# Optimization experiments

Measured on AMD Instinct MI355X. Metric: run time of the kernel, lower is better.

The kernel has to match this reference:

```python
import jax, jax.numpy as jnp
import numpy as np

N = 1_000_000       # total nodes
B = 4096            # number of graphs (batch_size)
D = 128             # in_channels
T = 3               # processing_steps
EPS = 1e-16         # torch_geometric softmax denominator epsilon


def setup_inputs() -> dict:
    key = jax.random.key(0)
    k0, k1, k2, k3, k4, k5 = jax.random.split(key, 6)
    x = jax.random.normal(k0, (N, D), dtype=jnp.float32)
    batch = jnp.sort(jax.random.randint(k1, (N,), 0, B, dtype=jnp.int32))
    # GRU params (input size 2D, hidden size D); scaled like orthogonal-ish init
    s = 1.0 / np.sqrt(D)
    w_ih = jax.random.normal(k2, (3 * D, 2 * D), dtype=jnp.float32) * s
    w_hh = jax.random.normal(k3, (3 * D, D), dtype=jnp.float32) * s
    b_ih = jax.random.normal(k4, (3 * D,), dtype=jnp.float32) * s
    b_hh = jax.random.normal(k5, (3 * D,), dtype=jnp.float32) * s
    return {"x": x, "batch": batch, "w_ih": w_ih, "w_hh": w_hh,
            "b_ih": b_ih, "b_hh": b_hh}


def _gru_cell(inp, h, w_ih, w_hh, b_ih, b_hh):
    # PyTorch GRU cell: gates ordered (r, z, n)
    gi = inp @ w_ih.T + b_ih          # [B, 3D]
    gh = h @ w_hh.T + b_hh            # [B, 3D]
    i_r, i_z, i_n = jnp.split(gi, 3, axis=-1)
    h_r, h_z, h_n = jnp.split(gh, 3, axis=-1)
    r = jax.nn.sigmoid(i_r + h_r)
    z = jax.nn.sigmoid(i_z + h_z)
    n = jnp.tanh(i_n + r * h_n)
    return (1.0 - z) * n + z * h


def reference(x, batch, w_ih, w_hh, b_ih, b_hh):
    h = jnp.zeros((B, D), dtype=x.dtype)
    q_star = jnp.zeros((B, 2 * D), dtype=x.dtype)
    for _ in range(T):  # small fixed number of processing steps
        h = _gru_cell(q_star, h, w_ih, w_hh, b_ih, b_hh)
        q = h                                           # [B, D]
        e = jnp.sum(x * q[batch], axis=-1)              # [N] dot scores
        # segment softmax over each graph's nodes
        m = jax.ops.segment_max(e, batch, num_segments=B)
        ex = jnp.exp(e - m[batch])
        s = jax.ops.segment_sum(ex, batch, num_segments=B)
        a = ex / (s[batch] + EPS)                       # [N]
        r_pool = jax.ops.segment_sum(a[:, None] * x, batch, num_segments=B)  # [B, D]
        q_star = jnp.concatenate([q, r_pool], axis=-1)  # [B, 2D]
    return q_star
```

## Files before the change

kernel.cpp:

```cpp
#include <hip/hip_runtime.h>
#include <hip/hip_bf16.h>
#include <math.h>

#define NB 4096
#define DD 128
#define TT 3

__global__ void transpose_w(const float* __restrict__ w, float* __restrict__ wt,
                            int R, int C) {
    int idx = blockIdx.x * blockDim.x + threadIdx.x;
    if (idx >= R * C) return;
    int r = idx % R;
    int c = idx / R;
    wt[idx] = w[r * C + c];
}

__global__ void seg_starts(const int* __restrict__ batch, int* __restrict__ seg,
                           int N, int B) {
    int i = blockIdx.x * blockDim.x + threadIdx.x;
    if (i >= N) return;
    int bi = batch[i];
    int bp = (i == 0) ? -1 : batch[i - 1];
    for (int b = bp + 1; b <= bi; ++b) seg[b] = i;
    if (i == N - 1) {
        for (int b = bi + 1; b <= B; ++b) seg[b] = N;
    }
}

__global__ __launch_bounds__(256) void gru_kernel(
    const float* qstar_in, const float* h_in,
    const float* __restrict__ wt_ih, const float* __restrict__ wt_hh,
    const float* __restrict__ b_ih, const float* __restrict__ b_hh,
    float* h_out, float* qstar_out ) {

    __shared__ float qs[16 * 256];
    __shared__ float hs[16 * 128];

    const int tid = threadIdx.x;
    const int b0  = blockIdx.x * 16;

    const float* qsrc = qstar_in + (size_t)b0 * 256;
    for (int t = tid; t < 16 * 256; t += 256) qs[t] = qsrc[t];
    const float* hsrc = h_in + (size_t)b0 * 128;
    for (int t = tid; t < 16 * 128; t += 256) hs[t] = hsrc[t];
    __syncthreads();

    const int j  = tid & 127;
    const int gb = (tid >> 7) * 8;

    float air[8], aiz[8], ain[8], ahr[8], ahz[8], ahn[8];
    const float br = b_ih[j], bz = b_ih[128 + j], bn = b_ih[256 + j];
    const float cr = b_hh[j], cz = b_hh[128 + j], cn = b_hh[256 + j];
#pragma unroll
    for (int g = 0; g < 8; ++g) {
        air[g] = br; aiz[g] = bz; ain[g] = bn;
        ahr[g] = cr; ahz[g] = cz; ahn[g] = cn;
    }

#pragma unroll 4
    for (int k = 0; k < 256; ++k) {
        const float wr = wt_ih[k * 384 + j];
        const float wz = wt_ih[k * 384 + 128 + j];
        const float wn = wt_ih[k * 384 + 256 + j];
#pragma unroll
        for (int g = 0; g < 8; ++g) {
            const float qv = qs[(gb + g) * 256 + k];
            air[g] = fmaf(qv, wr, air[g]);
            aiz[g] = fmaf(qv, wz, aiz[g]);
            ain[g] = fmaf(qv, wn, ain[g]);
        }
    }
#pragma unroll 4
    for (int k = 0; k < 128; ++k) {
        const float wr = wt_hh[k * 384 + j];
        const float wz = wt_hh[k * 384 + 128 + j];
        const float wn = wt_hh[k * 384 + 256 + j];
#pragma unroll
        for (int g = 0; g < 8; ++g) {
            const float hv = hs[(gb + g) * 128 + k];
            ahr[g] = fmaf(hv, wr, ahr[g]);
            ahz[g] = fmaf(hv, wz, ahz[g]);
            ahn[g] = fmaf(hv, wn, ahn[g]);
        }
    }

#pragma unroll
    for (int g = 0; g < 8; ++g) {
        const int gg = gb + g;
        const float r = 1.f / (1.f + __expf(-(air[g] + ahr[g])));
        const float z = 1.f / (1.f + __expf(-(aiz[g] + ahz[g])));
        const float n = tanhf(ain[g] + r * ahn[g]);
        const float hv = hs[gg * 128 + j];
        const float hnew = (1.f - z) * n + z * hv;
        const size_t row = (size_t)(b0 + gg);
        h_out[row * 128 + j]     = hnew;
        qstar_out[row * 256 + j] = hnew;
    }
}

__global__ __launch_bounds__(256) void attn_pool(
    const float* __restrict__ x, const float* __restrict__ h,
    const int* __restrict__ seg, float* qstar) {

    const int b   = blockIdx.x;
    const int tid = threadIdx.x;
    const int l   = tid & 31;
    const int grp = tid >> 5;

    __shared__ float  m_s[8];
    __shared__ float  s_s[8];
    __shared__ float4 acc_s[8][32];

    const int s0 = seg[b];
    const int s1 = seg[b + 1];

    if (s0 >= s1) {
        if (tid < 32) {
            float4 z4 = make_float4(0.f, 0.f, 0.f, 0.f);
            *(float4*)&qstar[(size_t)b * 256 + 128 + 4 * tid] = z4;
        }
        return;
    }

    const float4 qv = *(const float4*)&h[(size_t)b * 128 + 4 * l];

    float  m = -INFINITY;
    float  s = 0.f;
    float4 acc = make_float4(0.f, 0.f, 0.f, 0.f);

    for (int n = s0 + grp; n < s1; n += 8) {
        const float4 xv = *(const float4*)&x[(size_t)n * 128 + 4 * l];
        float d = xv.x * qv.x + xv.y * qv.y + xv.z * qv.z + xv.w * qv.w;
        d += __shfl_xor(d, 1);
        d += __shfl_xor(d, 2);
        d += __shfl_xor(d, 4);
        d += __shfl_xor(d, 8);
        d += __shfl_xor(d, 16);

        if (d <= m) {
            const float w = __expf(d - m);
            s += w;
            acc.x = fmaf(w, xv.x, acc.x);
            acc.y = fmaf(w, xv.y, acc.y);
            acc.z = fmaf(w, xv.z, acc.z);
            acc.w = fmaf(w, xv.w, acc.w);
        } else {
            const float c = __expf(m - d);
            s = fmaf(s, c, 1.f);
            acc.x = fmaf(acc.x, c, xv.x);
            acc.y = fmaf(acc.y, c, xv.y);
            acc.z = fmaf(acc.z, c, xv.z);
            acc.w = fmaf(acc.w, c, xv.w);
            m = d;
        }
    }

    if (l == 0) { m_s[grp] = m; s_s[grp] = s; }
    __syncthreads();

    float M = m_s[0];
#pragma unroll
    for (int g = 1; g < 8; ++g) M = fmaxf(M, m_s[g]);
    float stot = 0.f;
#pragma unroll
    for (int g = 0; g < 8; ++g) stot += s_s[g] * __expf(m_s[g] - M);

    const float f = __expf(m - M);
    acc.x *= f; acc.y *= f; acc.z *= f; acc.w *= f;
    acc_s[grp][l] = acc;
    __syncthreads();

    if (tid < 32) {
        float4 r = acc_s[0][tid];
#pragma unroll
        for (int g = 1; g < 8; ++g) {
            const float4 t4 = acc_s[g][tid];
            r.x += t4.x; r.y += t4.y; r.z += t4.z; r.w += t4.w;
        }
        const float inv = 1.f / (stot + 1e-16f);
        r.x *= inv; r.y *= inv; r.z *= inv; r.w *= inv;
        *(float4*)&qstar[(size_t)b * 256 + 128 + 4 * tid] = r;
    }
}

extern "C" void kernel_launch(void* const* d_in, const int* in_sizes, int n_in,
                              void* d_out, int out_size, void* d_ws, size_t ws_size,
                              hipStream_t stream) {
    const float* x     = (const float*)d_in[0];
    const int*   batch = (const int*)d_in[1];
    const float* w_ih  = (const float*)d_in[2];
    const float* w_hh  = (const float*)d_in[3];
    const float* b_ih  = (const float*)d_in[4];
    const float* b_hh  = (const float*)d_in[5];
    const int N = in_sizes[1];

    float* qstar = (float*)d_ws;
    float* h     = qstar + (size_t)NB * 256;
    float* wt_ih = h + (size_t)NB * 128;
    float* wt_hh = wt_ih + 256 * 384;
    int*   seg   = (int*)(wt_hh + 128 * 384);

    hipMemsetAsync(qstar, 0, (size_t)(NB * 256 + NB * 128) * sizeof(float), stream);

    transpose_w<<<(384 * 256 + 255) / 256, 256, 0, stream>>>(w_ih, wt_ih, 384, 256);
    transpose_w<<<(384 * 128 + 255) / 256, 256, 0, stream>>>(w_hh, wt_hh, 384, 128);
    seg_starts<<<(N + 255) / 256, 256, 0, stream>>>(batch, seg, N, NB);

    for (int t = 0; t < TT; ++t) {
        gru_kernel<<<NB / 16, 256, 0, stream>>>(qstar, h, wt_ih, wt_hh, b_ih, b_hh,
                                                h, qstar);
        attn_pool<<<NB, 256, 0, stream>>>(x, h, seg, qstar);
    }

    hipMemcpyAsync(d_out, qstar, (size_t)NB * 256 * sizeof(float),
                   hipMemcpyDeviceToDevice, stream);
}
```

Measured before the change: 1.028 ms.

## Process 32 nodes per block iteration with 8 lanes per node and prefetch

The attention-pool kernel now assigns 8 threads per node, each holding 64 bytes of the row, so a 256-thread block works on 32 nodes at once instead of 8. It adds a register double-buffer that loads the next node's row while the current one is processed. The online softmax becomes branchless through a running max with two exponentials. The aim is more memory-level parallelism and shorter shuffle reductions. In exchange it uses more registers and a larger shared-memory reduction across 32 partial accumulators.

```diff
diff --git a/kernel.cpp b/kernel.cpp
--- a/kernel.cpp
+++ b/kernel.cpp
@@ -100,86 +100,110 @@
 
 __global__ __launch_bounds__(256) void attn_pool(
     const float* __restrict__ x, const float* __restrict__ h,
-    const int* __restrict__ seg, float* qstar) {
+    const int* __restrict__ seg, float* __restrict__ qstar) {
 
     const int b   = blockIdx.x;
     const int tid = threadIdx.x;
-    const int l   = tid & 31;
-    const int grp = tid >> 5;
-
-    __shared__ float  m_s[8];
-    __shared__ float  s_s[8];
-    __shared__ float4 acc_s[8][32];
+    const int p   = tid & 7;
+    const int g   = tid >> 3;
+
+    __shared__ float m_s[32];
+    __shared__ float s_s[32];
+    __shared__ float acc_s[32][128];
 
     const int s0 = seg[b];
     const int s1 = seg[b + 1];
 
     if (s0 >= s1) {
         if (tid < 32) {
-            float4 z4 = make_float4(0.f, 0.f, 0.f, 0.f);
-            *(float4*)&qstar[(size_t)b * 256 + 128 + 4 * tid] = z4;
+            *(float4*)&qstar[(size_t)b * 256 + 128 + 4 * tid] =
+                make_float4(0.f, 0.f, 0.f, 0.f);
         }
         return;
     }
 
-    const float4 qv = *(const float4*)&h[(size_t)b * 128 + 4 * l];
-
-    float  m = -INFINITY;
-    float  s = 0.f;
-    float4 acc = make_float4(0.f, 0.f, 0.f, 0.f);
-
-    for (int n = s0 + grp; n < s1; n += 8) {
-        const float4 xv = *(const float4*)&x[(size_t)n * 128 + 4 * l];
-        float d = xv.x * qv.x + xv.y * qv.y + xv.z * qv.z + xv.w * qv.w;
+    const float* hb = h + (size_t)b * 128 + p * 16;
+    const float4 q0 = *(const float4*)(hb + 0);
+    const float4 q1 = *(const float4*)(hb + 4);
+    const float4 q2 = *(const float4*)(hb + 8);
+    const float4 q3 = *(const float4*)(hb + 12);
+
+    float m = -INFINITY, s = 0.f;
+    float4 a0 = make_float4(0,0,0,0), a1 = a0, a2 = a0, a3 = a0;
+
+    int n = s0 + g;
+    float4 c0, c1, c2, c3;
+    if (n < s1) {
+        const float* xb = x + (size_t)n * 128 + p * 16;
+        c0 = *(const float4*)(xb + 0);
+        c1 = *(const float4*)(xb + 4);
+        c2 = *(const float4*)(xb + 8);
+        c3 = *(const float4*)(xb + 12);
+    }
+
+    while (n < s1) {
+        const float4 d0 = c0, d1 = c1, d2 = c2, d3 = c3;
+        const int n2 = n + 32;
+        if (n2 < s1) {
+            const float* xb = x + (size_t)n2 * 128 + p * 16;
+            c0 = *(const float4*)(xb + 0);
+            c1 = *(const float4*)(xb + 4);
+            c2 = *(const float4*)(xb + 8);
+            c3 = *(const float4*)(xb + 12);
+        }
+
+        float d = d0.x*q0.x + d0.y*q0.y + d0.z*q0.z + d0.w*q0.w
+                + d1.x*q1.x + d1.y*q1.y + d1.z*q1.z + d1.w*q1.w
+                + d2.x*q2.x + d2.y*q2.y + d2.z*q2.z + d2.w*q2.w
+                + d3.x*q3.x + d3.y*q3.y + d3.z*q3.z + d3.w*q3.w;
         d += __shfl_xor(d, 1);
         d += __shfl_xor(d, 2);
         d += __shfl_xor(d, 4);
-        d += __shfl_xor(d, 8);
-        d += __shfl_xor(d, 16);
-
-        if (d <= m) {
-            const float w = __expf(d - m);
-            s += w;
-            acc.x = fmaf(w, xv.x, acc.x);
-            acc.y = fmaf(w, xv.y, acc.y);
-            acc.z = fmaf(w, xv.z, acc.z);
-            acc.w = fmaf(w, xv.w, acc.w);
-        } else {
-            const float c = __expf(m - d);
-            s = fmaf(s, c, 1.f);
-            acc.x = fmaf(acc.x, c, xv.x);
-            acc.y = fmaf(acc.y, c, xv.y);
-            acc.z = fmaf(acc.z, c, xv.z);
-            acc.w = fmaf(acc.w, c, xv.w);
-            m = d;
-        }
-    }
-
-    if (l == 0) { m_s[grp] = m; s_s[grp] = s; }
+
+        const float nm = fmaxf(m, d);
+        const float cs = __expf(m - nm);
+        const float w  = __expf(d - nm);
+        s = fmaf(s, cs, w);
+        a0.x = fmaf(a0.x, cs, w * d0.x); a0.y = fmaf(a0.y, cs, w * d0.y);
+        a0.z = fmaf(a0.z, cs, w * d0.z); a0.w = fmaf(a0.w, cs, w * d0.w);
+        a1.x = fmaf(a1.x, cs, w * d1.x); a1.y = fmaf(a1.y, cs, w * d1.y);
+        a1.z = fmaf(a1.z, cs, w * d1.z); a1.w = fmaf(a1.w, cs, w * d1.w);
+        a2.x = fmaf(a2.x, cs, w * d2.x); a2.y = fmaf(a2.y, cs, w * d2.y);
+        a2.z = fmaf(a2.z, cs, w * d2.z); a2.w = fmaf(a2.w, cs, w * d2.w);
+        a3.x = fmaf(a3.x, cs, w * d3.x); a3.y = fmaf(a3.y, cs, w * d3.y);
+        a3.z = fmaf(a3.z, cs, w * d3.z); a3.w = fmaf(a3.w, cs, w * d3.w);
+        m = nm;
+        n = n2;
+    }
+
+    if (p == 0) { m_s[g] = m; s_s[g] = s; }
     __syncthreads();
 
     float M = m_s[0];
 #pragma unroll
-    for (int g = 1; g < 8; ++g) M = fmaxf(M, m_s[g]);
-    float stot = 0.f;
-#pragma unroll
-    for (int g = 0; g < 8; ++g) stot += s_s[g] * __expf(m_s[g] - M);
-
-    const float f = __expf(m - M);
-    acc.x *= f; acc.y *= f; acc.z *= f; acc.w *= f;
-    acc_s[grp][l] = acc;
+    for (int i = 1; i < 32; ++i) M = fmaxf(M, m_s[i]);
+    float S = 0.f;
+#pragma unroll
+    for (int i = 0; i < 32; ++i) S += s_s[i] * __expf(m_s[i] - M);
+
+    const float f = __expf(m - M) / (S + 1e-16f);
+    a0.x *= f; a0.y *= f; a0.z *= f; a0.w *= f;
+    a1.x *= f; a1.y *= f; a1.z *= f; a1.w *= f;
+    a2.x *= f; a2.y *= f; a2.z *= f; a2.w *= f;
+    a3.x *= f; a3.y *= f; a3.z *= f; a3.w *= f;
+
+    float* row = &acc_s[g][p * 16];
+    *(float4*)(row + 0)  = a0;
+    *(float4*)(row + 4)  = a1;
+    *(float4*)(row + 8)  = a2;
+    *(float4*)(row + 12) = a3;
     __syncthreads();
 
-    if (tid < 32) {
-        float4 r = acc_s[0][tid];
-#pragma unroll
-        for (int g = 1; g < 8; ++g) {
-            const float4 t4 = acc_s[g][tid];
-            r.x += t4.x; r.y += t4.y; r.z += t4.z; r.w += t4.w;
-        }
-        const float inv = 1.f / (stot + 1e-16f);
-        r.x *= inv; r.y *= inv; r.z *= inv; r.w *= inv;
-        *(float4*)&qstar[(size_t)b * 256 + 128 + 4 * tid] = r;
+    if (tid < 128) {
+        float r = 0.f;
+#pragma unroll
+        for (int gg = 0; gg < 32; ++gg) r += acc_s[gg][tid];
+        qstar[(size_t)b * 256 + 128 + tid] = r;
     }
 }
 
```

Result: no change. 1.023 ms (-0.5%).

## Process four nodes per warp-group with register prefetch in attention pooling

Applied to the files above, without the earlier changes.

Each 32-lane group in attn_pool now handles four consecutive nodes per iteration. It keeps four independent online-softmax states and prefetches the next four x rows into registers before computing the current ones. This raises memory-level parallelism and interleaves the shuffle reductions, aimed at the latency-bound streaming of x. In exchange it uses more registers, computes two exps per node without branching, and wastes clamped loads on short segments (about 244 nodes per graph on average).

```diff
diff --git a/kernel.cpp b/kernel.cpp
--- a/kernel.cpp
+++ b/kernel.cpp
@@ -100,12 +100,12 @@
 
 __global__ __launch_bounds__(256) void attn_pool(
     const float* __restrict__ x, const float* __restrict__ h,
-    const int* __restrict__ seg, float* qstar) {
+    const int* __restrict__ seg, float* __restrict__ qstar) {
 
     const int b   = blockIdx.x;
     const int tid = threadIdx.x;
     const int l   = tid & 31;
-    const int grp = tid >> 5;
+    const int g   = tid >> 5;
 
     __shared__ float  m_s[8];
     __shared__ float  s_s[8];
@@ -116,69 +116,139 @@
 
     if (s0 >= s1) {
         if (tid < 32) {
-            float4 z4 = make_float4(0.f, 0.f, 0.f, 0.f);
-            *(float4*)&qstar[(size_t)b * 256 + 128 + 4 * tid] = z4;
+            *(float4*)&qstar[(size_t)b * 256 + 128 + 4 * tid] =
+                make_float4(0.f, 0.f, 0.f, 0.f);
         }
         return;
     }
 
     const float4 qv = *(const float4*)&h[(size_t)b * 128 + 4 * l];
-
-    float  m = -INFINITY;
-    float  s = 0.f;
-    float4 acc = make_float4(0.f, 0.f, 0.f, 0.f);
-
-    for (int n = s0 + grp; n < s1; n += 8) {
-        const float4 xv = *(const float4*)&x[(size_t)n * 128 + 4 * l];
-        float d = xv.x * qv.x + xv.y * qv.y + xv.z * qv.z + xv.w * qv.w;
-        d += __shfl_xor(d, 1);
-        d += __shfl_xor(d, 2);
-        d += __shfl_xor(d, 4);
-        d += __shfl_xor(d, 8);
-        d += __shfl_xor(d, 16);
-
-        if (d <= m) {
-            const float w = __expf(d - m);
-            s += w;
-            acc.x = fmaf(w, xv.x, acc.x);
-            acc.y = fmaf(w, xv.y, acc.y);
-            acc.z = fmaf(w, xv.z, acc.z);
-            acc.w = fmaf(w, xv.w, acc.w);
-        } else {
-            const float c = __expf(m - d);
-            s = fmaf(s, c, 1.f);
-            acc.x = fmaf(acc.x, c, xv.x);
-            acc.y = fmaf(acc.y, c, xv.y);
-            acc.z = fmaf(acc.z, c, xv.z);
-            acc.w = fmaf(acc.w, c, xv.w);
-            m = d;
-        }
-    }
-
-    if (l == 0) { m_s[grp] = m; s_s[grp] = s; }
+    const int len = s1 - s0;
+    const int nt  = (len + 31) >> 5;
+
+    float m0 = -1e30f, m1 = -1e30f, m2 = -1e30f, m3 = -1e30f;
+    float sA = 0.f, sB = 0.f, sC = 0.f, sD = 0.f;
+    float4 a0 = make_float4(0,0,0,0), a1 = a0, a2 = a0, a3 = a0;
+
+    int base = s0 + g * 4;
+    const int last = s1 - 1;
+
+    float4 c0, c1, c2, c3;
+    {
+        c0 = *(const float4*)&x[(size_t)min(base + 0, last) * 128 + 4 * l];
+        c1 = *(const float4*)&x[(size_t)min(base + 1, last) * 128 + 4 * l];
+        c2 = *(const float4*)&x[(size_t)min(base + 2, last) * 128 + 4 * l];
+        c3 = *(const float4*)&x[(size_t)min(base + 3, last) * 128 + 4 * l];
+    }
+
+    for (int j = 0; j < nt; ++j) {
+        const float4 d0 = c0, d1 = c1, d2 = c2, d3 = c3;
+        const int nb = base + 32;
+        if (j + 1 < nt) {
+            c0 = *(const float4*)&x[(size_t)min(nb + 0, last) * 128 + 4 * l];
+            c1 = *(const float4*)&x[(size_t)min(nb + 1, last) * 128 + 4 * l];
+            c2 = *(const float4*)&x[(size_t)min(nb + 2, last) * 128 + 4 * l];
+            c3 = *(const float4*)&x[(size_t)min(nb + 3, last) * 128 + 4 * l];
+        }
+
+        float e0 = d0.x*qv.x + d0.y*qv.y + d0.z*qv.z + d0.w*qv.w;
+        float e1 = d1.x*qv.x + d1.y*qv.y + d1.z*qv.z + d1.w*qv.w;
+        float e2 = d2.x*qv.x + d2.y*qv.y + d2.z*qv.z + d2.w*qv.w;
+        float e3 = d3.x*qv.x + d3.y*qv.y + d3.z*qv.z + d3.w*qv.w;
+#pragma unroll
+        for (int o = 1; o < 32; o <<= 1) {
+            e0 += __shfl_xor(e0, o);
+            e1 += __shfl_xor(e1, o);
+            e2 += __shfl_xor(e2, o);
+            e3 += __shfl_xor(e3, o);
+        }
+        e0 = (base + 0 < s1) ? e0 : -3e38f;
+        e1 = (base + 1 < s1) ? e1 : -3e38f;
+        e2 = (base + 2 < s1) ? e2 : -3e38f;
+        e3 = (base + 3 < s1) ? e3 : -3e38f;
+
+        {
+            const float nm = fmaxf(m0, e0);
+            const float cs = __expf(m0 - nm), w = __expf(e0 - nm);
+            sA = fmaf(sA, cs, w);
+            a0.x = fmaf(a0.x, cs, w * d0.x); a0.y = fmaf(a0.y, cs, w * d0.y);
+            a0.z = fmaf(a0.z, cs, w * d0.z); a0.w = fmaf(a0.w, cs, w * d0.w);
+            m0 = nm;
+        }
+        {
+            const float nm = fmaxf(m1, e1);
+            const float cs = __expf(m1 - nm), w = __expf(e1 - nm);
+            sB = fmaf(sB, cs, w);
+            a1.x = fmaf(a1.x, cs, w * d1.x); a1.y = fmaf(a1.y, cs, w * d1.y);
+            a1.z = fmaf(a1.z, cs, w * d1.z); a1.w = fmaf(a1.w, cs, w * d1.w);
+            m1 = nm;
+        }
+        {
+            const float nm = fmaxf(m2, e2);
+            const float cs = __expf(m2 - nm), w = __expf(e2 - nm);
+            sC = fmaf(sC, cs, w);
+            a2.x = fmaf(a2.x, cs, w * d2.x); a2.y = fmaf(a2.y, cs, w * d2.y);
+            a2.z = fmaf(a2.z, cs, w * d2.z); a2.w = fmaf(a2.w, cs, w * d2.w);
+            m2 = nm;
+        }
+        {
+            const float nm = fmaxf(m3, e3);
+            const float cs = __expf(m3 - nm), w = __expf(e3 - nm);
+            sD = fmaf(sD, cs, w);
+            a3.x = fmaf(a3.x, cs, w * d3.x); a3.y = fmaf(a3.y, cs, w * d3.y);
+            a3.z = fmaf(a3.z, cs, w * d3.z); a3.w = fmaf(a3.w, cs, w * d3.w);
+            m3 = nm;
+        }
+        base = nb;
+    }
+
+    {
+        const float M = fmaxf(m0, m1);
+        const float f0 = __expf(m0 - M), f1 = __expf(m1 - M);
+        sA = sA * f0 + sB * f1;
+        a0.x = a0.x*f0 + a1.x*f1; a0.y = a0.y*f0 + a1.y*f1;
+        a0.z = a0.z*f0 + a1.z*f1; a0.w = a0.w*f0 + a1.w*f1;
+        m0 = M;
+    }
+    {
+        const float M = fmaxf(m2, m3);
+        const float f2 = __expf(m2 - M), f3 = __expf(m3 - M);
+        sC = sC * f2 + sD * f3;
+        a2.x = a2.x*f2 + a3.x*f3; a2.y = a2.y*f2 + a3.y*f3;
+        a2.z = a2.z*f2 + a3.z*f3; a2.w = a2.w*f2 + a3.w*f3;
+        m2 = M;
+    }
+    {
+        const float M = fmaxf(m0, m2);
+        const float f0 = __expf(m0 - M), f2 = __expf(m2 - M);
+        sA = sA * f0 + sC * f2;
+        a0.x = a0.x*f0 + a2.x*f2; a0.y = a0.y*f0 + a2.y*f2;
+        a0.z = a0.z*f0 + a2.z*f2; a0.w = a0.w*f0 + a2.w*f2;
+        m0 = M;
+    }
+
+    if (l == 0) { m_s[g] = m0; s_s[g] = sA; }
     __syncthreads();
 
     float M = m_s[0];
 #pragma unroll
-    for (int g = 1; g < 8; ++g) M = fmaxf(M, m_s[g]);
-    float stot = 0.f;
-#pragma unroll
-    for (int g = 0; g < 8; ++g) stot += s_s[g] * __expf(m_s[g] - M);
-
-    const float f = __expf(m - M);
-    acc.x *= f; acc.y *= f; acc.z *= f; acc.w *= f;
-    acc_s[grp][l] = acc;
+    for (int i = 1; i < 8; ++i) M = fmaxf(M, m_s[i]);
+    float S = 0.f;
+#pragma unroll
+    for (int i = 0; i < 8; ++i) S += s_s[i] * __expf(m_s[i] - M);
+
+    const float f = __expf(m0 - M) / (S + 1e-16f);
+    a0.x *= f; a0.y *= f; a0.z *= f; a0.w *= f;
+    acc_s[g][l] = a0;
     __syncthreads();
 
     if (tid < 32) {
         float4 r = acc_s[0][tid];
 #pragma unroll
-        for (int g = 1; g < 8; ++g) {
-            const float4 t4 = acc_s[g][tid];
+        for (int gg = 1; gg < 8; ++gg) {
+            const float4 t4 = acc_s[gg][tid];
             r.x += t4.x; r.y += t4.y; r.z += t4.z; r.w += t4.w;
         }
-        const float inv = 1.f / (stot + 1e-16f);
-        r.x *= inv; r.y *= inv; r.z *= inv; r.w *= inv;
         *(float4*)&qstar[(size_t)b * 256 + 128 + 4 * tid] = r;
     }
 }
```

After: 1.022 ms. Within noise of the previous version (-0.6%).
